# Kernel optimization log

Measured on AMD Instinct MI355X. Metric: run time of the kernel, lower is better.

Reference implementation:

```python
import jax, jax.numpy as jnp
import numpy as np
from jax import lax

# Config (matches init_kwargs / ModelCfg.__post_init__)
B, L = 2, 1024
D, E, N, D_DELTA, D_CONV, V, N_LAYERS = 768, 1536, 16, 48, 4, 50280, 2


def setup_inputs() -> dict:
    key = jax.random.key(0)
    ks = jax.random.split(key, 16)
    s = 0.02
    inp = {
        "tokens": jax.random.randint(ks[0], (B, L), 0, V),
        "embedding": jax.random.normal(ks[1], (V, D), jnp.float32) * s,
        "norm_w": jnp.ones((N_LAYERS, D), jnp.float32),
        "skip_w": jax.random.normal(ks[2], (N_LAYERS, E, D), jnp.float32) * s,
        "in_w": jax.random.normal(ks[3], (N_LAYERS, E, D), jnp.float32) * s,
        "conv_w": jax.random.normal(ks[4], (N_LAYERS, E, 1, D_CONV), jnp.float32) * 0.1,
        "conv_b": jax.random.normal(ks[5], (N_LAYERS, E), jnp.float32) * s,
        "Wd1": jax.random.normal(ks[6], (N_LAYERS, D_DELTA, E), jnp.float32) * s,
        "Wd2_w": jax.random.normal(ks[7], (N_LAYERS, E, D_DELTA), jnp.float32) * s,
        "Wd2_b": jax.random.normal(ks[8], (N_LAYERS, E), jnp.float32) * s,
        "WB": jax.random.normal(ks[9], (N_LAYERS, N, E), jnp.float32) * s,
        "WC": jax.random.normal(ks[10], (N_LAYERS, N, E), jnp.float32) * s,
        "A_log": jax.random.normal(ks[11], (N_LAYERS, E, N), jnp.float32) * 0.5,
        "W_D": jnp.ones((N_LAYERS, E), jnp.float32),
        "out_w": jax.random.normal(ks[12], (N_LAYERS, D, E), jnp.float32) * s,
        "final_norm_w": jnp.ones((D,), jnp.float32),
        "lm_head_w": jax.random.normal(ks[13], (V, D), jnp.float32) * s,
    }
    return inp


def rmsnorm(x, w, eps=1e-5):
    return x * lax.rsqrt(jnp.mean(x * x, axis=-1, keepdims=True) + eps) * w


def mamba_block(resid, nw, skw, inw, cw, cb, wd1, wd2w, wd2b, wb, wc, a_log, wd, ow):
    x = rmsnorm(resid, nw)                      # [B,L,D]
    skip = x @ skw.T                            # [B,L,E]
    xi = x @ inw.T                              # [B,L,E]
    # depthwise causal conv1d (left pad D_CONV-1 == torch pad + slice [:L])
    xc = lax.conv_general_dilated(
        xi.transpose(0, 2, 1), cw, window_strides=(1,),
        padding=[(D_CONV - 1, 0)], feature_group_count=E,
        dimension_numbers=("NCH", "OIH", "NCH"))
    x = jax.nn.silu((xc + cb[None, :, None]).transpose(0, 2, 1))  # [B,L,E]

    A = -jnp.exp(a_log)                                            # [E,N]
    delta = jax.nn.softplus((x @ wd1.T) @ wd2w.T + wd2b)           # [B,L,E]
    Bm = x @ wb.T                                                  # [B,L,N]
    Cm = x @ wc.T                                                  # [B,L,N]
    dA = jnp.exp(delta[..., None] * A)                             # [B,L,E,N]
    dBx = delta[..., None] * Bm[:, :, None, :] * x[..., None]      # [B,L,E,N]

    def step(h, t):
        dA_t, dBx_t, C_t = t
        h = dA_t * h + dBx_t                                       # [B,E,N]
        y = jnp.einsum("ben,bn->be", h, C_t)
        return h, y

    h0 = jnp.zeros((B, E, N), x.dtype)
    _, ys = lax.scan(step, h0, (dA.transpose(1, 0, 2, 3),
                                dBx.transpose(1, 0, 2, 3),
                                Cm.transpose(1, 0, 2)))
    y = ys.transpose(1, 0, 2)                                      # [B,L,E]
    y = (y + x * wd) * jax.nn.silu(skip)
    return resid + y @ ow.T


def reference(tokens, embedding, norm_w, skip_w, in_w, conv_w, conv_b, Wd1,
              Wd2_w, Wd2_b, WB, WC, A_log, W_D, out_w, final_norm_w, lm_head_w):
    resid = embedding[tokens]                                      # [B,L,D]
    for i in range(N_LAYERS):
        resid = mamba_block(resid, norm_w[i], skip_w[i], in_w[i], conv_w[i],
                            conv_b[i], Wd1[i], Wd2_w[i], Wd2_b[i], WB[i],
                            WC[i], A_log[i], W_D[i], out_w[i])
    resid = rmsnorm(resid, final_norm_w)
    logits = resid @ lm_head_w.T                                   # [B,L,V]
    return logits
```

## Files before the change

kernel.cpp:

```cpp
#include <hip/hip_runtime.h>
#include <hip/hip_bf16.h>

#define BB     2
#define LL     1024
#define BL     (BB*LL)
#define BDIM   768
#define EDIM   1536
#define NST    16
#define DDELTA 48
#define DDPAD  64
#define DCONV  4
#define VOCAB  50280
#define NLAYERS 2

#define CCH    16
#define TCH    (LL/CCH)
#define BEN    (BB*EDIM*NST)

typedef __hip_bfloat16 bf16;
typedef short short8 __attribute__((ext_vector_type(8)));
typedef float floatx4 __attribute__((ext_vector_type(4)));

static __device__ __forceinline__ float bf2f(bf16 v){ return __bfloat162float(v); }
static __device__ __forceinline__ bf16  f2bf(float v){ return __float2bfloat16(v); }

__global__ void k_cvt(const float* __restrict__ src, bf16* __restrict__ dst) {
  int idx = blockIdx.x*256 + threadIdx.x;
  dst[idx] = f2bf(src[idx]);
}

__global__ void k_embed(const int* __restrict__ tok, const float* __restrict__ emb,
                        float* __restrict__ resid) {
  int idx = blockIdx.x*256 + threadIdx.x;
  int bl = idx / BDIM, d = idx % BDIM;
  resid[idx] = emb[(size_t)tok[bl]*BDIM + d];
}

__global__ __launch_bounds__(256) void k_rmsnorm(const float* __restrict__ resid,
                        const float* __restrict__ w, bf16* __restrict__ out) {
  int m = blockIdx.x, tid = threadIdx.x;
  const float* row = resid + (size_t)m*BDIM;
  float ss = 0.f;
  for (int d = tid; d < BDIM; d += 256) { float v = row[d]; ss += v*v; }
  for (int off = 32; off; off >>= 1) ss += __shfl_down(ss, off);
  __shared__ float red[4];
  if ((tid & 63) == 0) red[tid>>6] = ss;
  __syncthreads();
  float rstd = rsqrtf((red[0]+red[1]+red[2]+red[3]) / (float)BDIM + 1e-5f);
  for (int d = tid; d < BDIM; d += 256)
    out[(size_t)m*BDIM + d] = f2bf(row[d]*rstd*w[d]);
}

template<bool OUT_BF16>
__global__ __launch_bounds__(256) void k_gemm(const bf16* __restrict__ A,
      const bf16* __restrict__ W, void* __restrict__ Cp, int N, int K) {
  __shared__ alignas(16) bf16 As[128*32];
  __shared__ alignas(16) bf16 Bs[128*32];
  const int m0 = blockIdx.y * 128, n0 = blockIdx.x * 128;
  const int tid = threadIdx.x, lane = tid & 63, wave = tid >> 6;
  const int wm = (wave >> 1) * 64, wn = (wave & 1) * 64;
  const int r = tid >> 2, c = tid & 3;
  const int mr = lane & 15, q = lane >> 4;
  floatx4 acc[4][4] = {};

  int wr0 = n0 + r;       if (wr0 >= N) wr0 = N - 1;
  int wr1 = n0 + 64 + r;  if (wr1 >= N) wr1 = N - 1;

  for (int k0 = 0; k0 < K; k0 += 32) {
    int4 a0 = *reinterpret_cast<const int4*>(A + (size_t)(m0 + r     )*K + k0 + c*8);
    int4 a1 = *reinterpret_cast<const int4*>(A + (size_t)(m0 + 64 + r)*K + k0 + c*8);
    int4 b0 = *reinterpret_cast<const int4*>(W + (size_t)wr0*K + k0 + c*8);
    int4 b1 = *reinterpret_cast<const int4*>(W + (size_t)wr1*K + k0 + c*8);
    __syncthreads();
    *reinterpret_cast<int4*>(&As[(r     )*32 + c*8]) = a0;
    *reinterpret_cast<int4*>(&As[(64 + r)*32 + c*8]) = a1;
    *reinterpret_cast<int4*>(&Bs[(r     )*32 + c*8]) = b0;
    *reinterpret_cast<int4*>(&Bs[(64 + r)*32 + c*8]) = b1;
    __syncthreads();
    short8 af[4], bfr[4];
    #pragma unroll
    for (int i = 0; i < 4; i++)
      af[i]  = *reinterpret_cast<const short8*>(&As[(wm + i*16 + mr)*32 + q*8]);
    #pragma unroll
    for (int j = 0; j < 4; j++)
      bfr[j] = *reinterpret_cast<const short8*>(&Bs[(wn + j*16 + mr)*32 + q*8]);
    #pragma unroll
    for (int i = 0; i < 4; i++)
      #pragma unroll
      for (int j = 0; j < 4; j++)
        acc[i][j] = __builtin_amdgcn_mfma_f32_16x16x32_bf16(af[i], bfr[j], acc[i][j], 0, 0, 0);
  }
  #pragma unroll
  for (int i = 0; i < 4; i++)
    #pragma unroll
    for (int j = 0; j < 4; j++)
      #pragma unroll
      for (int rg = 0; rg < 4; rg++) {
        int m = m0 + wm + i*16 + q*4 + rg;
        int n = n0 + wn + j*16 + mr;
        if (n < N) {
          float v = acc[i][j][rg];
          if (OUT_BF16) ((bf16*)Cp)[(size_t)m*N + n] = f2bf(v);
          else          ((float*)Cp)[(size_t)m*N + n] = v;
        }
      }
}

__global__ void k_conv(const float* __restrict__ xi, const float* __restrict__ cw,
                       const float* __restrict__ cb, float* __restrict__ xc) {
  int idx = blockIdx.x*256 + threadIdx.x;
  int e = idx % EDIM, bl = idx / EDIM, l = bl % LL;
  float acc = cb[e];
  #pragma unroll
  for (int k = 0; k < DCONV; k++) {
    int ls = l - (DCONV-1) + k;
    if (ls >= 0) acc += xi[(size_t)(bl + ls - l)*EDIM + e] * cw[e*DCONV + k];
  }
  xc[idx] = acc / (1.f + expf(-acc));
}

__global__ __launch_bounds__(256) void k_d1(const float* __restrict__ xc,
      const float* __restrict__ wd1, bf16* __restrict__ d1) {
  int m = blockIdx.x, tid = threadIdx.x;
  __shared__ float xrow[EDIM];
  for (int k = tid; k < EDIM; k += 256) xrow[k] = xc[(size_t)m*EDIM + k];
  __syncthreads();
  int wave = tid >> 6, lane = tid & 63;
  for (int n = wave; n < DDPAD; n += 4) {
    float s = 0.f;
    if (n < DDELTA) {
      const float* wr = wd1 + (size_t)n*EDIM;
      for (int k = lane; k < EDIM; k += 64) s += xrow[k]*wr[k];
      for (int off = 32; off; off >>= 1) s += __shfl_down(s, off);
    }
    if (lane == 0) d1[(size_t)m*DDPAD + n] = f2bf(s);
  }
}

__global__ void k_padw(const float* __restrict__ wsrc, bf16* __restrict__ wp) {
  int idx = blockIdx.x*256 + threadIdx.x;
  int e = idx >> 6, cc = idx & 63;
  wp[idx] = (cc < DDELTA) ? f2bf(wsrc[(size_t)e*DDELTA + cc]) : f2bf(0.f);
}

__global__ void k_softplus(float* __restrict__ d, const float* __restrict__ b) {
  int idx = blockIdx.x*256 + threadIdx.x;
  int e = idx % EDIM;
  float v = d[idx] + b[e];
  d[idx] = fmaxf(v, 0.f) + log1pf(expf(-fabsf(v)));
}

__global__ __launch_bounds__(256) void k_bc(const float* __restrict__ xc,
    const float* __restrict__ wb, const float* __restrict__ wc,
    float* __restrict__ Bm, float* __restrict__ Cm) {
  int m = blockIdx.x, tid = threadIdx.x;
  __shared__ float xrow[EDIM];
  for (int k = tid; k < EDIM; k += 256) xrow[k] = xc[(size_t)m*EDIM + k];
  __syncthreads();
  int wave = tid >> 6, lane = tid & 63;
  for (int n = wave; n < 32; n += 4) {
    const float* wr = (n < NST) ? wb + (size_t)n*EDIM : wc + (size_t)(n-NST)*EDIM;
    float s = 0.f;
    for (int k = lane; k < EDIM; k += 64) s += xrow[k]*wr[k];
    for (int off = 32; off; off >>= 1) s += __shfl_down(s, off);
    if (lane == 0) {
      if (n < NST) Bm[(size_t)m*NST + n]       = s;
      else         Cm[(size_t)m*NST + (n-NST)] = s;
    }
  }
}



__global__ __launch_bounds__(256) void k_scan1(const float* __restrict__ delta,
    const float* __restrict__ xc, const float* __restrict__ Bm,
    const float* __restrict__ a_log, float* __restrict__ Pbuf,
    float* __restrict__ Hbuf) {
  int tid = threadIdx.x;
  int n = tid & 15, el = tid >> 4;
  int bx = blockIdx.x;
  int et = bx % (EDIM/16); bx /= (EDIM/16);
  int c = bx % CCH, b = bx / CCH;
  int e = et*16 + el;
  float Aen = -__expf(a_log[(size_t)e*NST + n]);
  const float* dp = delta + ((size_t)b*LL + (size_t)c*TCH)*EDIM + e;
  const float* xp = xc    + ((size_t)b*LL + (size_t)c*TCH)*EDIM + e;
  const float* bp = Bm    + ((size_t)b*LL + (size_t)c*TCH)*NST + n;
  float h = 0.f, p = 1.f;
  #pragma unroll 4
  for (int t = 0; t < TCH; t++) {
    float dl = dp[(size_t)t*EDIM];
    float xv = xp[(size_t)t*EDIM];
    float bv = bp[t*NST];
    float a = __expf(dl*Aen);
    h = a*h + dl*bv*xv;
    p *= a;
  }
  size_t ben = ((size_t)b*EDIM + e)*NST + n;
  Pbuf[(size_t)c*BEN + ben] = p;
  Hbuf[(size_t)c*BEN + ben] = h;
}

__global__ __launch_bounds__(256) void k_scanfix(const float* __restrict__ Pbuf,
    const float* __restrict__ Hbuf, float* __restrict__ Hin) {
  int ben = blockIdx.x*256 + threadIdx.x;
  float h = 0.f;
  #pragma unroll
  for (int c = 0; c < CCH; c++) {
    Hin[(size_t)c*BEN + ben] = h;
    h = Pbuf[(size_t)c*BEN + ben]*h + Hbuf[(size_t)c*BEN + ben];
  }
}

__global__ __launch_bounds__(256) void k_scan2(const float* __restrict__ delta,
    const float* __restrict__ xc, const float* __restrict__ Bm,
    const float* __restrict__ Cm, const float* __restrict__ a_log,
    const float* __restrict__ Hin, float* __restrict__ y) {
  int tid = threadIdx.x;
  int n = tid & 15, el = tid >> 4;
  int bx = blockIdx.x;
  int et = bx % (EDIM/16); bx /= (EDIM/16);
  int c = bx % CCH, b = bx / CCH;
  int e = et*16 + el;
  float Aen = -__expf(a_log[(size_t)e*NST + n]);
  const float* dp = delta + ((size_t)b*LL + (size_t)c*TCH)*EDIM + e;
  const float* xp = xc    + ((size_t)b*LL + (size_t)c*TCH)*EDIM + e;
  const float* bp = Bm    + ((size_t)b*LL + (size_t)c*TCH)*NST + n;
  const float* cp = Cm    + ((size_t)b*LL + (size_t)c*TCH)*NST + n;
  float* yp = y + ((size_t)b*LL + (size_t)c*TCH)*EDIM + e;
  size_t ben = ((size_t)b*EDIM + e)*NST + n;
  float h = Hin[(size_t)c*BEN + ben];
  #pragma unroll 4
  for (int t = 0; t < TCH; t++) {
    float dl = dp[(size_t)t*EDIM];
    float xv = xp[(size_t)t*EDIM];
    float bv = bp[t*NST];
    float cv = cp[t*NST];
    h = __expf(dl*Aen)*h + dl*bv*xv;
    float p = h*cv;
    p += __shfl_xor(p, 1); p += __shfl_xor(p, 2);
    p += __shfl_xor(p, 4); p += __shfl_xor(p, 8);
    if (n == 0) yp[(size_t)t*EDIM] = p;
  }
}

__global__ void k_ymix(const float* __restrict__ y, const float* __restrict__ xc,
    const float* __restrict__ skip, const float* __restrict__ wd, bf16* __restrict__ y2) {
  int idx = blockIdx.x*256 + threadIdx.x;
  int e = idx % EDIM;
  float s = skip[idx];
  y2[idx] = f2bf((y[idx] + xc[idx]*wd[e]) * (s / (1.f + expf(-s))));
}

__global__ void k_add(float* __restrict__ resid, const float* __restrict__ d) {
  int idx = blockIdx.x*256 + threadIdx.x;
  resid[idx] += d[idx];
}

extern "C" void kernel_launch(void* const* d_in, const int* in_sizes, int n_in,
                              void* d_out, int out_size, void* d_ws, size_t ws_size,
                              hipStream_t stream) {
  const int*   tokens = (const int*)  d_in[0];
  const float* emb    = (const float*)d_in[1];
  const float* norm_w = (const float*)d_in[2];
  const float* skip_w = (const float*)d_in[3];
  const float* in_w   = (const float*)d_in[4];
  const float* conv_w = (const float*)d_in[5];
  const float* conv_b = (const float*)d_in[6];
  const float* Wd1    = (const float*)d_in[7];
  const float* Wd2w   = (const float*)d_in[8];
  const float* Wd2b   = (const float*)d_in[9];
  const float* WBw    = (const float*)d_in[10];
  const float* WCw    = (const float*)d_in[11];
  const float* A_log  = (const float*)d_in[12];
  const float* W_D    = (const float*)d_in[13];
  const float* out_w  = (const float*)d_in[14];
  const float* fnw    = (const float*)d_in[15];
  const float* lm_w   = (const float*)d_in[16];
  float* out = (float*)d_out;

  char* wsp = (char*)d_ws;
  auto alloc = [&](size_t bytes) { char* p = wsp; wsp += (bytes + 255) & ~(size_t)255; return p; };
  float* resid = (float*)alloc((size_t)BL*BDIM*4);
  bf16*  xn    = (bf16*) alloc((size_t)BL*BDIM*2);
  float* skip  = (float*)alloc((size_t)BL*EDIM*4);
  float* xi    = (float*)alloc((size_t)BL*EDIM*4);
  float* xc    = (float*)alloc((size_t)BL*EDIM*4);
  float* dlt   = (float*)alloc((size_t)BL*EDIM*4);
  bf16*  d1    = (bf16*) alloc((size_t)BL*DDPAD*2);
  bf16*  w2p   = (bf16*) alloc((size_t)EDIM*DDPAD*2);
  float* Bm    = (float*)alloc((size_t)BL*NST*4);
  float* Cm    = (float*)alloc((size_t)BL*NST*4);
  bf16*  y2    = (bf16*) alloc((size_t)BL*EDIM*2);
  float* Pbuf  = (float*)alloc((size_t)CCH*BEN*4);
  float* Hbuf  = (float*)alloc((size_t)CCH*BEN*4);
  float* Hin   = (float*)alloc((size_t)CCH*BEN*4);
  bf16*  wcvt  = (bf16*) alloc((size_t)VOCAB*BDIM*2);

  dim3 blk(256);
  const int nED = EDIM*BDIM/256;
  const int scanGrid = BB*CCH*(EDIM/16);
  k_embed<<<BL*BDIM/256, blk, 0, stream>>>(tokens, emb, resid);
  for (int l = 0; l < NLAYERS; l++) {
    k_rmsnorm<<<BL, blk, 0, stream>>>(resid, norm_w + (size_t)l*BDIM, xn);

    k_cvt<<<nED, blk, 0, stream>>>(skip_w + (size_t)l*EDIM*BDIM, wcvt);
    k_gemm<false><<<dim3(EDIM/128, BL/128), blk, 0, stream>>>(xn, wcvt, skip, EDIM, BDIM);

    k_cvt<<<nED, blk, 0, stream>>>(in_w + (size_t)l*EDIM*BDIM, wcvt);
    k_gemm<false><<<dim3(EDIM/128, BL/128), blk, 0, stream>>>(xn, wcvt, xi, EDIM, BDIM);

    k_conv<<<BL*EDIM/256, blk, 0, stream>>>(
        xi, conv_w + (size_t)l*EDIM*DCONV, conv_b + (size_t)l*EDIM, xc);
    k_d1<<<BL, blk, 0, stream>>>(xc, Wd1 + (size_t)l*DDELTA*EDIM, d1);
    k_padw<<<EDIM*DDPAD/256, blk, 0, stream>>>(Wd2w + (size_t)l*EDIM*DDELTA, w2p);
    k_gemm<false><<<dim3(EDIM/128, BL/128), blk, 0, stream>>>(d1, w2p, dlt, EDIM, DDPAD);
    k_softplus<<<BL*EDIM/256, blk, 0, stream>>>(dlt, Wd2b + (size_t)l*EDIM);
    k_bc<<<BL, blk, 0, stream>>>(xc, WBw + (size_t)l*NST*EDIM, WCw + (size_t)l*NST*EDIM, Bm, Cm);

    k_scan1<<<scanGrid, blk, 0, stream>>>(dlt, xc, Bm,
        A_log + (size_t)l*EDIM*NST, Pbuf, Hbuf);
    k_scanfix<<<BEN/256, blk, 0, stream>>>(Pbuf, Hbuf, Hin);
    k_scan2<<<scanGrid, blk, 0, stream>>>(dlt, xc, Bm, Cm,
        A_log + (size_t)l*EDIM*NST, Hin, xi);

    k_ymix<<<BL*EDIM/256, blk, 0, stream>>>(xi, xc, skip, W_D + (size_t)l*EDIM, y2);

    k_cvt<<<nED, blk, 0, stream>>>(out_w + (size_t)l*BDIM*EDIM, wcvt);
    k_gemm<false><<<dim3(BDIM/128, BL/128), blk, 0, stream>>>(
        y2, wcvt, dlt, BDIM, EDIM);
    k_add<<<BL*BDIM/256, blk, 0, stream>>>(resid, dlt);
  }
  k_rmsnorm<<<BL, blk, 0, stream>>>(resid, fnw, xn);
  k_cvt<<<VOCAB*BDIM/256, blk, 0, stream>>>(lm_w, wcvt);
  k_gemm<false><<<dim3((VOCAB+127)/128, BL/128), blk, 0, stream>>>(
      xn, wcvt, out, VOCAB, BDIM);
}
```

Measured before the change: 1.667 ms.

## Load GEMM tiles directly to LDS and remap workgroups across XCDs

The GEMM's global-to-register-to-LDS staging is replaced by global_load_lds direct-to-LDS transfers of 16 bytes per lane, each wave filling its own contiguous row slab. Block indices are also remapped so consecutive logical tiles land on the same XCD, which is meant to improve L2 reuse of shared A/W rows. The intent is fewer VGPRs and LDS-store instructions, but the loop still waits on vmcnt(0) with a single buffer, so there is no overlap of load and compute.

```diff
diff --git a/kernel.cpp b/kernel.cpp
--- a/kernel.cpp
+++ b/kernel.cpp
@@ -23,6 +23,12 @@
 
 static __device__ __forceinline__ float bf2f(bf16 v){ return __bfloat162float(v); }
 static __device__ __forceinline__ bf16  f2bf(float v){ return __float2bfloat16(v); }
+
+typedef const __attribute__((address_space(1))) unsigned int gu32;
+typedef __attribute__((address_space(3))) unsigned int lu32;
+static __device__ __forceinline__ void glds16(const bf16* g, bf16* l) {
+  __builtin_amdgcn_global_load_lds((gu32*)g, (lu32*)l, 16, 0, 0);
+}
 
 __global__ void k_cvt(const float* __restrict__ src, bf16* __restrict__ dst) {
   int idx = blockIdx.x*256 + threadIdx.x;
@@ -56,26 +62,40 @@
       const bf16* __restrict__ W, void* __restrict__ Cp, int N, int K) {
   __shared__ alignas(16) bf16 As[128*32];
   __shared__ alignas(16) bf16 Bs[128*32];
-  const int m0 = blockIdx.y * 128, n0 = blockIdx.x * 128;
+  const int nwg = gridDim.x * gridDim.y;
+  const int orig = blockIdx.y * gridDim.x + blockIdx.x;
+  const int qq = nwg >> 3, rr = nwg & 7;
+  const int xcd = orig & 7, sub = orig >> 3;
+  const int logical = (xcd < rr ? xcd*(qq+1) : rr*(qq+1) + (xcd-rr)*qq) + sub;
+  const int by = logical % gridDim.y;
+  const int bx = logical / gridDim.y;
+  const int m0 = by * 128, n0 = bx * 128;
+
   const int tid = threadIdx.x, lane = tid & 63, wave = tid >> 6;
   const int wm = (wave >> 1) * 64, wn = (wave & 1) * 64;
-  const int r = tid >> 2, c = tid & 3;
   const int mr = lane & 15, q = lane >> 4;
   floatx4 acc[4][4] = {};
 
-  int wr0 = n0 + r;       if (wr0 >= N) wr0 = N - 1;
-  int wr1 = n0 + 64 + r;  if (wr1 >= N) wr1 = N - 1;
+  const int sr = lane >> 2, ch = lane & 3;
+  const int wbase = wave * 16;
+  int wr0 = n0 + wbase + sr;      if (wr0 >= N) wr0 = N - 1;
+  int wr1 = n0 + 64 + wbase + sr; if (wr1 >= N) wr1 = N - 1;
+  const bf16* Ar0 = A + (size_t)(m0 + wbase + sr)*K      + ch*8;
+  const bf16* Ar1 = A + (size_t)(m0 + 64 + wbase + sr)*K + ch*8;
+  const bf16* Wr0 = W + (size_t)wr0*K + ch*8;
+  const bf16* Wr1 = W + (size_t)wr1*K + ch*8;
+  bf16* lA0 = As + wbase*32;
+  bf16* lA1 = As + (64 + wbase)*32;
+  bf16* lB0 = Bs + wbase*32;
+  bf16* lB1 = Bs + (64 + wbase)*32;
 
   for (int k0 = 0; k0 < K; k0 += 32) {
-    int4 a0 = *reinterpret_cast<const int4*>(A + (size_t)(m0 + r     )*K + k0 + c*8);
-    int4 a1 = *reinterpret_cast<const int4*>(A + (size_t)(m0 + 64 + r)*K + k0 + c*8);
-    int4 b0 = *reinterpret_cast<const int4*>(W + (size_t)wr0*K + k0 + c*8);
-    int4 b1 = *reinterpret_cast<const int4*>(W + (size_t)wr1*K + k0 + c*8);
     __syncthreads();
-    *reinterpret_cast<int4*>(&As[(r     )*32 + c*8]) = a0;
-    *reinterpret_cast<int4*>(&As[(64 + r)*32 + c*8]) = a1;
-    *reinterpret_cast<int4*>(&Bs[(r     )*32 + c*8]) = b0;
-    *reinterpret_cast<int4*>(&Bs[(64 + r)*32 + c*8]) = b1;
+    glds16(Ar0 + k0, lA0);
+    glds16(Ar1 + k0, lA1);
+    glds16(Wr0 + k0, lB0);
+    glds16(Wr1 + k0, lB1);
+    asm volatile("s_waitcnt vmcnt(0)" ::: "memory");
     __syncthreads();
     short8 af[4], bfr[4];
     #pragma unroll
@@ -169,7 +189,6 @@
     }
   }
 }
-
 
 
 __global__ __launch_bounds__(256) void k_scan1(const float* __restrict__ delta,
```

Result: no change. 1.664 ms (-0.1%).
